# Kernel optimization log

Measured on AMD Instinct MI355X. Metric: run time of the kernel, lower is better.

The kernel has to match this reference:

```python
import jax, jax.numpy as jnp
import numpy as np
import math

D_MODEL = 1024
NUM_HEADS = 16
HEAD_DIM = D_MODEL // NUM_HEADS  # 64


def setup_inputs() -> dict:
    key = jax.random.key(0)
    ks = jax.random.split(key, 5)
    B, T = 4, 2048
    scale = 1.0 / math.sqrt(D_MODEL)
    return {
        "x": jax.random.normal(ks[0], (B, T, D_MODEL), dtype=jnp.float32),
        "wq": jax.random.normal(ks[1], (D_MODEL, D_MODEL), dtype=jnp.float32) * scale,
        "wk": jax.random.normal(ks[2], (D_MODEL, D_MODEL), dtype=jnp.float32) * scale,
        "wv": jax.random.normal(ks[3], (D_MODEL, D_MODEL), dtype=jnp.float32) * scale,
        "wo": jax.random.normal(ks[4], (D_MODEL, D_MODEL), dtype=jnp.float32) * scale,
    }


def reference(x, wq, wk, wv, wo):
    B, T, _ = x.shape
    H, Dk = NUM_HEADS, HEAD_DIM

    def split_heads(t):  # [B,T,D] -> [B,H,T,Dk]
        return t.reshape(B, T, H, Dk).transpose(0, 2, 1, 3)

    q = split_heads(x @ wq)
    k = split_heads(x @ wk)
    v = split_heads(x @ wv)

    # scaled QK^T: [B,H,T,T]
    scores = jnp.einsum("bhqd,bhkd->bhqk", q, k) / jnp.sqrt(jnp.float32(Dk))
    # causal mask: triu(ones, diag=0).T.bool() == lower-triangular incl. diagonal
    causal = jnp.tril(jnp.ones((T, T), dtype=bool))
    scores = jnp.where(causal, scores, -jnp.inf)
    attn = jax.nn.softmax(scores, axis=-1)

    out = jnp.einsum("bhqk,bhkd->bhqd", attn, v)  # [B,H,T,Dk]
    out = out.transpose(0, 2, 1, 3).reshape(B, T, H * Dk)
    return out @ wo
```

## Files before the change

### kernel.cpp

```cpp
#include <hip/hip_runtime.h>
#include <hip/hip_bf16.h>
#include <stdint.h>

typedef __attribute__((ext_vector_type(8))) short bf16x8;
typedef __attribute__((ext_vector_type(4))) float f32x4;
typedef __attribute__((ext_vector_type(4))) unsigned short u16x4;
typedef __attribute__((ext_vector_type(4))) float float4v;

#define MFMA16(a, b, c) __builtin_amdgcn_mfma_f32_16x16x32_bf16((a), (b), (c), 0, 0, 0)

__device__ __forceinline__ unsigned short f2bf(float f) {
  union { float f; uint32_t u; } v; v.f = f;
  uint32_t r = (v.u + 0x7FFFu + ((v.u >> 16) & 1u)) >> 16;
  return (unsigned short)r;
}

typedef const __attribute__((address_space(1))) void* gptr1_t;
typedef __attribute__((address_space(3))) void* lptr3_t;
__device__ __forceinline__ void gload16(const void* g, void* l) {
  __builtin_amdgcn_global_load_lds((gptr1_t)g, (lptr3_t)l, 16, 0, 0);
}

__global__ __launch_bounds__(256) void cvt_x_kernel(const float* __restrict__ in,
                                                    unsigned short* __restrict__ out) {
  int i = blockIdx.x * 256 + threadIdx.x;
  float4v f = ((const float4v*)in)[i];
  u16x4 o;
  o[0] = f2bf(f[0]); o[1] = f2bf(f[1]); o[2] = f2bf(f[2]); o[3] = f2bf(f[3]);
  ((u16x4*)out)[i] = o;
}

__global__ __launch_bounds__(256) void wt_cvt_kernel(const float* __restrict__ w0,
                                                     const float* __restrict__ w1,
                                                     const float* __restrict__ w2,
                                                     const float* __restrict__ w3,
                                                     unsigned short* __restrict__ out) {
  const float* in = blockIdx.z == 0 ? w0 : blockIdx.z == 1 ? w1 : blockIdx.z == 2 ? w2 : w3;
  unsigned short* o = out + (size_t)blockIdx.z * 1024 * 1024;
  __shared__ float tile[32][33];
  int tx = threadIdx.x & 31, ty = threadIdx.x >> 5;
  int c0 = blockIdx.x * 32, r0 = blockIdx.y * 32;
#pragma unroll
  for (int i = 0; i < 4; i++)
    tile[ty + 8 * i][tx] = in[(size_t)(r0 + ty + 8 * i) * 1024 + c0 + tx];
  __syncthreads();
#pragma unroll
  for (int i = 0; i < 4; i++)
    o[(size_t)(c0 + ty + 8 * i) * 1024 + r0 + tx] = f2bf(tile[tx][ty + 8 * i]);
}

template <bool OUTF32>
__global__ __launch_bounds__(256) void gemm128_kernel(
    const unsigned short* __restrict__ A,
    const unsigned short* __restrict__ B0, const unsigned short* __restrict__ B1,
    const unsigned short* __restrict__ B2,
    void* C0, void* C1, void* C2) {
  constexpr int K = 1024, N = 1024;
  const unsigned short* Bt = blockIdx.z == 0 ? B0 : blockIdx.z == 1 ? B1 : B2;
  void* Cv = blockIdx.z == 0 ? C0 : blockIdx.z == 1 ? C1 : C2;

  __shared__ unsigned short As[128 * 32];
  __shared__ unsigned short Bs[128 * 32];

  const int tid = threadIdx.x;
  const int w = tid >> 6, lane = tid & 63, l15 = lane & 15, l4 = lane >> 4;
  const int wm = w >> 1, wn = w & 1;
  const int m0 = blockIdx.x * 128, n0 = blockIdx.y * 128;

  f32x4 acc[4][4] = {};

  const int srow = w * 32 + (lane >> 2);
  const int scol = (lane & 3) * 8;
  const unsigned short* ga = A + (size_t)(m0 + srow) * K + scol;
  const unsigned short* gb = Bt + (size_t)(n0 + srow) * K + scol;
  char* lA = (char*)As + w * 2048;
  char* lB = (char*)Bs + w * 2048;

  for (int k0 = 0; k0 < K; k0 += 32) {
    __syncthreads();
    gload16(ga + k0, lA);
    gload16(ga + k0 + 16 * K, lA + 1024);
    gload16(gb + k0, lB);
    gload16(gb + k0 + 16 * K, lB + 1024);
    __syncthreads();

    bf16x8 af[4], bfr[4];
#pragma unroll
    for (int mi = 0; mi < 4; mi++)
      af[mi] = *(const bf16x8*)&As[(wm * 64 + mi * 16 + l15) * 32 + 8 * l4];
#pragma unroll
    for (int ni = 0; ni < 4; ni++)
      bfr[ni] = *(const bf16x8*)&Bs[(wn * 64 + ni * 16 + l15) * 32 + 8 * l4];
#pragma unroll
    for (int mi = 0; mi < 4; mi++)
#pragma unroll
      for (int ni = 0; ni < 4; ni++)
        acc[mi][ni] = MFMA16(af[mi], bfr[ni], acc[mi][ni]);
  }

#pragma unroll
  for (int mi = 0; mi < 4; mi++)
#pragma unroll
    for (int ni = 0; ni < 4; ni++)
#pragma unroll
      for (int r = 0; r < 4; r++) {
        int mg = m0 + wm * 64 + mi * 16 + 4 * l4 + r;
        int ng = n0 + wn * 64 + ni * 16 + l15;
        if (OUTF32)
          ((float*)Cv)[(size_t)mg * N + ng] = acc[mi][ni][r];
        else
          ((unsigned short*)Cv)[(size_t)mg * N + ng] = f2bf(acc[mi][ni][r]);
      }
}

__global__ __launch_bounds__(256, 4) void attn_kernel(const unsigned short* __restrict__ Qb,
                                                      const unsigned short* __restrict__ Kb,
                                                      const unsigned short* __restrict__ Vb,
                                                      unsigned short* __restrict__ Ob) {
  const int p = blockIdx.x, h = blockIdx.y, bb = blockIdx.z;
  const int tid = threadIdx.x, w = tid >> 6, lane = tid & 63, l15 = lane & 15, l4 = lane >> 4;

  __shared__ unsigned short K_lds[2][64 * 64];
  __shared__ unsigned short Vt_lds[2][64 * 64];
  __shared__ unsigned short P_lds[4][16 * 64];

  const size_t brow = (size_t)bb * 2048;
  const int qq = w * 16 + l15;
  const int sw = 8 * (l15 & 7);
  constexpr float C = 0.18033688f;

  const int qbA = p, qbB = 31 - p;
  const int lastB = qbB;

  bf16x8 qfA0, qfA1, qfB0, qfB1;
  {
    const unsigned short* qa = Qb + (brow + qbA * 64 + qq) * 1024 + h * 64 + 8 * l4;
    qfA0 = *(const bf16x8*)qa;
    qfA1 = *(const bf16x8*)(qa + 32);
    const unsigned short* qbp = Qb + (brow + qbB * 64 + qq) * 1024 + h * 64 + 8 * l4;
    qfB0 = *(const bf16x8*)qbp;
    qfB1 = *(const bf16x8*)(qbp + 32);
  }

  f32x4 oA[4] = {}, oB[4] = {};
  float mrA = -__builtin_inff(), lrA = 0.0f;
  float mrB = -__builtin_inff(), lrB = 0.0f;

  const int kcol = 8 * ((lane & 7) ^ ((lane >> 3) & 7));
  const unsigned short* gk = Kb + (brow + 8 * w + (lane >> 3)) * 1024 + h * 64 + kcol;
  const int vr0 = 2 * (tid >> 3);
  const int vsc = (tid & 7) * 8;
  const unsigned short* gv = Vb + (brow + vr0) * 1024 + h * 64 + vsc;

  auto vt_write = [&](int buf, const bf16x8& v0, const bf16x8& v1) {
#pragma unroll
    for (int j = 0; j < 8; j++) {
      const int d = vsc + j;
      const int msk = 8 * ((d ^ (d >> 3)) & 7);
      uint32_t pk = (uint32_t)(unsigned short)v0[j] |
                    ((uint32_t)(unsigned short)v1[j] << 16);
      *(uint32_t*)&Vt_lds[buf][d * 64 + (vr0 ^ msk)] = pk;
    }
  };

  auto tile_compute = [&](const unsigned short* Kc, const unsigned short* Vtc,
                          const bf16x8& q0f, const bf16x8& q1f, f32x4* oacc,
                          float& m_run, float& l_run, bool diag) {
    f32x4 s[4];
    __builtin_amdgcn_s_setprio(1);
#pragma unroll
    for (int sub = 0; sub < 4; ++sub) {
      const unsigned short* kr0 = &Kc[(sub * 16 + l15) * 64 + ((8 * l4) ^ sw)];
      const unsigned short* kr1 = &Kc[(sub * 16 + l15) * 64 + ((32 + 8 * l4) ^ sw)];
      f32x4 z = {0.f, 0.f, 0.f, 0.f};
      z = MFMA16(*(const bf16x8*)kr0, q0f, z);
      z = MFMA16(*(const bf16x8*)kr1, q1f, z);
      s[sub] = z;
    }
    __builtin_amdgcn_s_setprio(0);

    float mt = -__builtin_inff();
    if (diag) {
#pragma unroll
      for (int sub = 0; sub < 4; ++sub)
#pragma unroll
        for (int r4 = 0; r4 < 4; r4++) {
          const int kv_t = sub * 16 + 4 * l4 + r4;
          float sv = s[sub][r4];
          sv = (kv_t > qq) ? -__builtin_inff() : sv;
          s[sub][r4] = sv;
          mt = fmaxf(mt, sv);
        }
    } else {
#pragma unroll
      for (int sub = 0; sub < 4; ++sub)
#pragma unroll
        for (int r4 = 0; r4 < 4; r4++) mt = fmaxf(mt, s[sub][r4]);
    }
    mt = fmaxf(mt, __shfl_xor(mt, 16));
    mt = fmaxf(mt, __shfl_xor(mt, 32));

    float m_new = m_run;
    if (!__all(mt <= m_run + 44.3614f)) {
      m_new = fmaxf(m_run, mt);
      const float alpha = __builtin_amdgcn_exp2f((m_run - m_new) * C);
      const float ao0 = __shfl(alpha, 4 * l4 + 0);
      const float ao1 = __shfl(alpha, 4 * l4 + 1);
      const float ao2 = __shfl(alpha, 4 * l4 + 2);
      const float ao3 = __shfl(alpha, 4 * l4 + 3);
#pragma unroll
      for (int d = 0; d < 4; ++d) {
        oacc[d][0] *= ao0; oacc[d][1] *= ao1; oacc[d][2] *= ao2; oacc[d][3] *= ao3;
      }
      l_run *= alpha;
      m_run = m_new;
    }
    const float mnc = m_new * C;

    float lt = 0.0f;
#pragma unroll
    for (int sub = 0; sub < 4; ++sub) {
      u16x4 pw;
#pragma unroll
      for (int r4 = 0; r4 < 4; r4++) {
        float pv = __builtin_amdgcn_exp2f(__builtin_fmaf(s[sub][r4], C, -mnc));
        lt += pv;
        pw[r4] = f2bf(pv);
      }
      *(u16x4*)&P_lds[w][l15 * 64 + ((sub * 16 + 4 * l4) ^ sw)] = pw;
    }
    lt += __shfl_xor(lt, 16);
    lt += __shfl_xor(lt, 32);
    l_run += lt;

    const bf16x8 pf0 = *(const bf16x8*)&P_lds[w][l15 * 64 + ((8 * l4) ^ sw)];
    const bf16x8 pf1 = *(const bf16x8*)&P_lds[w][l15 * 64 + ((32 + 8 * l4) ^ sw)];
    __builtin_amdgcn_s_setprio(1);
#pragma unroll
    for (int d = 0; d < 4; ++d) {
      const int dd = d * 16 + l15;
      const int vm = 8 * ((dd ^ (dd >> 3)) & 7);
      const unsigned short* vp0 = &Vtc[dd * 64 + ((8 * l4) ^ vm)];
      const unsigned short* vp1 = &Vtc[dd * 64 + ((32 + 8 * l4) ^ vm)];
      oacc[d] = MFMA16(pf0, *(const bf16x8*)vp0, oacc[d]);
      oacc[d] = MFMA16(pf1, *(const bf16x8*)vp1, oacc[d]);
    }
    __builtin_amdgcn_s_setprio(0);
  };

  gload16(gk, (char*)K_lds[0] + w * 1024);
  gload16(gk + 32 * 1024, (char*)K_lds[0] + w * 1024 + 4096);
  {
    bf16x8 v0 = *(const bf16x8*)gv;
    bf16x8 v1 = *(const bf16x8*)(gv + 1024);
    vt_write(0, v0, v1);
  }
  __syncthreads();

  for (int kb = 0; kb <= lastB; ++kb) {
    const int cur = kb & 1, nxt = cur ^ 1;
    const bool pre = kb < lastB;
    bf16x8 pv0, pv1;
    if (pre) {
      const size_t off = (size_t)(kb + 1) * 64 * 1024;
      gload16(gk + off, (char*)K_lds[nxt] + w * 1024);
      gload16(gk + off + 32 * 1024, (char*)K_lds[nxt] + w * 1024 + 4096);
      pv0 = *(const bf16x8*)(gv + off);
      pv1 = *(const bf16x8*)(gv + off + 1024);
    }

    if (kb <= qbA)
      tile_compute(K_lds[cur], Vt_lds[cur], qfA0, qfA1, oA, mrA, lrA, kb == qbA);
    tile_compute(K_lds[cur], Vt_lds[cur], qfB0, qfB1, oB, mrB, lrB, kb == lastB);

    if (pre) vt_write(nxt, pv0, pv1);
    __syncthreads();
  }

  {
    const float linv = 1.0f / lrA;
    const float li[4] = {__shfl(linv, 4 * l4 + 0), __shfl(linv, 4 * l4 + 1),
                         __shfl(linv, 4 * l4 + 2), __shfl(linv, 4 * l4 + 3)};
#pragma unroll
    for (int d = 0; d < 4; ++d)
#pragma unroll
      for (int r4 = 0; r4 < 4; r4++) {
        const size_t orow = brow + qbA * 64 + w * 16 + 4 * l4 + r4;
        Ob[orow * 1024 + h * 64 + d * 16 + l15] = f2bf(oA[d][r4] * li[r4]);
      }
  }
  {
    const float linv = 1.0f / lrB;
    const float li[4] = {__shfl(linv, 4 * l4 + 0), __shfl(linv, 4 * l4 + 1),
                         __shfl(linv, 4 * l4 + 2), __shfl(linv, 4 * l4 + 3)};
#pragma unroll
    for (int d = 0; d < 4; ++d)
#pragma unroll
      for (int r4 = 0; r4 < 4; r4++) {
        const size_t orow = brow + qbB * 64 + w * 16 + 4 * l4 + r4;
        Ob[orow * 1024 + h * 64 + d * 16 + l15] = f2bf(oB[d][r4] * li[r4]);
      }
  }
}

extern "C" void kernel_launch(void* const* d_in, const int* in_sizes, int n_in,
                              void* d_out, int out_size, void* d_ws, size_t ws_size,
                              hipStream_t stream) {
  const float* x  = (const float*)d_in[0];
  const float* wq = (const float*)d_in[1];
  const float* wk = (const float*)d_in[2];
  const float* wv = (const float*)d_in[3];
  const float* wo = (const float*)d_in[4];

  char* ws = (char*)d_ws;
  unsigned short* Xb  = (unsigned short*)(ws);
  unsigned short* Wt  = (unsigned short*)(ws + (16u << 20));
  unsigned short* Wqt = Wt;
  unsigned short* Wkt = Wt + (1u << 20);
  unsigned short* Wvt = Wt + (2u << 20);
  unsigned short* Wot = Wt + (3u << 20);
  unsigned short* Qb  = (unsigned short*)(ws + (24u << 20));
  unsigned short* Kb  = (unsigned short*)(ws + (40u << 20));
  unsigned short* Vb  = (unsigned short*)(ws + (56u << 20));
  unsigned short* Ob  = Xb;

  cvt_x_kernel<<<8192, 256, 0, stream>>>(x, Xb);
  wt_cvt_kernel<<<dim3(32, 32, 4), 256, 0, stream>>>(wq, wk, wv, wo, Wt);
  gemm128_kernel<false><<<dim3(64, 8, 3), 256, 0, stream>>>(Xb, Wqt, Wkt, Wvt, Qb, Kb, Vb);
  attn_kernel<<<dim3(16, 16, 4), 256, 0, stream>>>(Qb, Kb, Vb, Ob);
  gemm128_kernel<true><<<dim3(64, 8, 1), 256, 0, stream>>>(Ob, Wot, Wot, Wot, d_out, d_out, d_out);
}
```

Measured before the change: 185.2 us.

## Add 64-row output GEMM, XCD-aware attention block mapping, hardware bf16 convert

Several changes land together. The float-to-bf16 conversion now uses the compiler's __bf16 cast instead of manual integer rounding. The attention grid becomes 1D and is remapped so that all blocks for one (batch, head) pair fall on the same XCD, which should improve L2 reuse of K/V. The row-sum shuffle reduction moves after the PV MFMAs so it can overlap with them. The output projection switches to a new 64x128-tile GEMM with twice as many blocks, which improves occupancy on the 1024x... problem but uses a simple single-buffered K loop with two barriers per step.

```diff
diff --git a/kernel.cpp b/kernel.cpp
--- a/kernel.cpp
+++ b/kernel.cpp
@@ -10,9 +10,7 @@
 #define MFMA16(a, b, c) __builtin_amdgcn_mfma_f32_16x16x32_bf16((a), (b), (c), 0, 0, 0)
 
 __device__ __forceinline__ unsigned short f2bf(float f) {
-  union { float f; uint32_t u; } v; v.f = f;
-  uint32_t r = (v.u + 0x7FFFu + ((v.u >> 16) & 1u)) >> 16;
-  return (unsigned short)r;
+  return __builtin_bit_cast(unsigned short, (__bf16)f);
 }
 
 typedef const __attribute__((address_space(1))) void* gptr1_t;
@@ -113,11 +111,71 @@
       }
 }
 
+__global__ __launch_bounds__(256) void gemm64_kernel(const unsigned short* __restrict__ A,
+                                                     const unsigned short* __restrict__ Bt,
+                                                     float* __restrict__ Cv) {
+  constexpr int K = 1024, N = 1024;
+  __shared__ unsigned short As[64 * 32];
+  __shared__ unsigned short Bs[128 * 32];
+
+  const int tid = threadIdx.x;
+  const int w = tid >> 6, lane = tid & 63, l15 = lane & 15, l4 = lane >> 4;
+  const int wm = w >> 1, wn = w & 1;
+  const int m0 = blockIdx.x * 64, n0 = blockIdx.y * 128;
+
+  f32x4 acc[2][4] = {};
+
+  const int arow = w * 16 + (lane >> 2);
+  const int brow = w * 32 + (lane >> 2);
+  const int scol = (lane & 3) * 8;
+  const unsigned short* ga = A + (size_t)(m0 + arow) * K + scol;
+  const unsigned short* gb = Bt + (size_t)(n0 + brow) * K + scol;
+  char* lA = (char*)As + w * 1024;
+  char* lB = (char*)Bs + w * 2048;
+
+  for (int k0 = 0; k0 < K; k0 += 32) {
+    __syncthreads();
+    gload16(ga + k0, lA);
+    gload16(gb + k0, lB);
+    gload16(gb + k0 + 16 * K, lB + 1024);
+    __syncthreads();
+
+    bf16x8 af[2], bfr[4];
+#pragma unroll
+    for (int mi = 0; mi < 2; mi++)
+      af[mi] = *(const bf16x8*)&As[(wm * 32 + mi * 16 + l15) * 32 + 8 * l4];
+#pragma unroll
+    for (int ni = 0; ni < 4; ni++)
+      bfr[ni] = *(const bf16x8*)&Bs[(wn * 64 + ni * 16 + l15) * 32 + 8 * l4];
+#pragma unroll
+    for (int mi = 0; mi < 2; mi++)
+#pragma unroll
+      for (int ni = 0; ni < 4; ni++)
+        acc[mi][ni] = MFMA16(af[mi], bfr[ni], acc[mi][ni]);
+  }
+
+#pragma unroll
+  for (int mi = 0; mi < 2; mi++)
+#pragma unroll
+    for (int ni = 0; ni < 4; ni++)
+#pragma unroll
+      for (int r = 0; r < 4; r++) {
+        int mg = m0 + wm * 32 + mi * 16 + 4 * l4 + r;
+        int ng = n0 + wn * 64 + ni * 16 + l15;
+        Cv[(size_t)mg * N + ng] = acc[mi][ni][r];
+      }
+}
+
 __global__ __launch_bounds__(256, 4) void attn_kernel(const unsigned short* __restrict__ Qb,
                                                       const unsigned short* __restrict__ Kb,
                                                       const unsigned short* __restrict__ Vb,
                                                       unsigned short* __restrict__ Ob) {
-  const int p = blockIdx.x, h = blockIdx.y, bb = blockIdx.z;
+  const int bid = blockIdx.x;
+  const int xcd = bid & 7, slot = bid >> 3;
+  const int hb = xcd * 8 + (slot >> 4);
+  const int p = slot & 15;
+  const int h = hb & 15, bb = hb >> 4;
+
   const int tid = threadIdx.x, w = tid >> 6, lane = tid & 63, l15 = lane & 15, l4 = lane >> 4;
 
   __shared__ unsigned short K_lds[2][64 * 64];
@@ -229,9 +287,6 @@
       }
       *(u16x4*)&P_lds[w][l15 * 64 + ((sub * 16 + 4 * l4) ^ sw)] = pw;
     }
-    lt += __shfl_xor(lt, 16);
-    lt += __shfl_xor(lt, 32);
-    l_run += lt;
 
     const bf16x8 pf0 = *(const bf16x8*)&P_lds[w][l15 * 64 + ((8 * l4) ^ sw)];
     const bf16x8 pf1 = *(const bf16x8*)&P_lds[w][l15 * 64 + ((32 + 8 * l4) ^ sw)];
@@ -246,6 +301,10 @@
       oacc[d] = MFMA16(pf1, *(const bf16x8*)vp1, oacc[d]);
     }
     __builtin_amdgcn_s_setprio(0);
+
+    lt += __shfl_xor(lt, 16);
+    lt += __shfl_xor(lt, 32);
+    l_run += lt;
   };
 
   gload16(gk, (char*)K_lds[0] + w * 1024);
@@ -327,6 +386,6 @@
   cvt_x_kernel<<<8192, 256, 0, stream>>>(x, Xb);
   wt_cvt_kernel<<<dim3(32, 32, 4), 256, 0, stream>>>(wq, wk, wv, wo, Wt);
   gemm128_kernel<false><<<dim3(64, 8, 3), 256, 0, stream>>>(Xb, Wqt, Wkt, Wvt, Qb, Kb, Vb);
-  attn_kernel<<<dim3(16, 16, 4), 256, 0, stream>>>(Qb, Kb, Vb, Ob);
-  gemm128_kernel<true><<<dim3(64, 8, 1), 256, 0, stream>>>(Ob, Wot, Wot, Wot, d_out, d_out, d_out);
-}
+  attn_kernel<<<1024, 256, 0, stream>>>(Qb, Kb, Vb, Ob);
+  gemm64_kernel<<<dim3(128, 8), 256, 0, stream>>>(Ob, Wot, (float*)d_out);
+}
```

After: 175.0 us. 5.5% less time.
